# Kernel tuning notes

Measured on AMD Instinct MI355X. Metric: run time of the kernel, lower is better.

Reference implementation:

```python
import jax, jax.numpy as jnp
import numpy as np

B_, L_, DM = 2, 2048, 768        # batch, seq_len, d_model
DS, DC, EXP = 32, 7, 2           # d_state, d_conv, expand
DI = EXP * DM                    # d_inner = 1536
EPS = 1e-5


def setup_inputs() -> dict:
    key = jax.random.key(0)
    ks = jax.random.split(key, 6)
    sc = lambda k, shp: jax.random.normal(k, shp, jnp.float32) * 0.02
    x = jax.random.normal(ks[0], (B_, L_, DM), jnp.float32)
    Win = sc(ks[1], (2 * DI, DM))            # in_proj weight (no bias)
    conv_w = sc(ks[2], (DI, 1, DC))          # depthwise conv weight (O, I/groups, K)
    conv_b = jnp.zeros((DI,), jnp.float32)   # conv bias
    Wx = sc(ks[3], (2 * DS + DI, DI))        # x_proj weight (no bias)
    A_log = jnp.broadcast_to(jnp.log(jnp.arange(1, DS + 1, dtype=jnp.float32)), (DI, DS))
    D = jnp.ones((DI,), jnp.float32)
    Wout = sc(ks[4], (DM, DI))               # out_proj weight (no bias)
    ln_g = jnp.ones((DM,), jnp.float32)
    ln_b = jnp.zeros((DM,), jnp.float32)
    return {"x": x, "Win": Win, "conv_w": conv_w, "conv_b": conv_b, "Wx": Wx,
            "A_log": A_log, "D": D, "Wout": Wout, "ln_g": ln_g, "ln_b": ln_b}


def _mamba_forward(x, Win, conv_w, conv_b, Wx, A_log, D, Wout, ln_g, ln_b):
    residual = x
    # LayerNorm (biased variance, eps=1e-5)
    mu = jnp.mean(x, axis=-1, keepdims=True)
    var = jnp.var(x, axis=-1, keepdims=True)
    xn = (x - mu) / jnp.sqrt(var + EPS) * ln_g + ln_b
    # in_proj then split into x, z streams
    xz = xn @ Win.T                          # (b, l, 2*di)
    xc, z = jnp.split(xz, 2, axis=-1)
    # depthwise causal conv: pad (d_conv-1) left, truncate to L (matches torch pad+slice)
    xt = jnp.moveaxis(xc, 1, 2)              # (b, di, l)
    conv = jax.lax.conv_general_dilated(
        xt, conv_w, window_strides=(1,), padding=[(DC - 1, 0)],
        dimension_numbers=('NCH', 'OIH', 'NCH'), feature_group_count=DI)
    conv = conv + conv_b[None, :, None]
    xc = jax.nn.silu(jnp.moveaxis(conv, 1, 2))   # (b, l, di); dropout is identity (eval)
    # selective SSM
    xp = xc @ Wx.T                           # (b, l, 2*ds + di)
    Bm = xp[..., :DS]                        # (b, l, ds)
    Cm = xp[..., DS:2 * DS]                  # (b, l, ds)
    delta = jax.nn.softplus(xp[..., 2 * DS:])  # (b, l, di)
    A = -jnp.exp(A_log)                      # (di, ds)
    dA = jnp.exp(delta[..., None] * A)                       # (b, l, di, ds)
    dBx = (delta * xc)[..., None] * Bm[:, :, None, :]        # (b, l, di, ds)
    def step(h, inp):
        dA_t, dBx_t, C_t = inp
        h = dA_t * h + dBx_t                 # (b, di, ds)
        y = jnp.einsum('bdn,bn->bd', h, C_t)
        return h, y
    h0 = jnp.zeros((x.shape[0], DI, DS), xc.dtype)
    xs = (jnp.moveaxis(dA, 1, 0), jnp.moveaxis(dBx, 1, 0), jnp.moveaxis(Cm, 1, 0))
    _, ys = jax.lax.scan(step, h0, xs)       # (l, b, di)
    y = jnp.moveaxis(ys, 0, 1) + xc * D      # (b, l, di)
    # gated output, out_proj, residual
    y = y * jax.nn.silu(z)
    return y @ Wout.T + residual


def reference(x, Win, conv_w, conv_b, Wx, A_log, D, Wout, ln_g, ln_b):
    return _mamba_forward(x, Win, conv_w, conv_b, Wx, A_log, D, Wout, ln_g, ln_b)
```

## Files before the change

kernel.cpp:

```cpp
#include <hip/hip_runtime.h>
#include <hip/hip_bf16.h>

#define B_  2
#define L_  2048
#define DM  768
#define DS  32
#define DC  7
#define DI  1536
#define NTOK (B_*L_)
#define N1  (2*DI)
#define N2  (2*DS+DI)
#define N2P 1664
#define NC  64
#define CL  (L_/NC)
#define DGRP (DI/256)

using bf16 = __hip_bfloat16;
typedef short  short8 __attribute__((ext_vector_type(8)));
typedef short  s16x4  __attribute__((ext_vector_type(4)));
typedef float  f32x4  __attribute__((ext_vector_type(4)));
typedef unsigned u32x4 __attribute__((ext_vector_type(4)));

__device__ __forceinline__ float b2f(bf16 h) { return __bfloat162float(h); }
__device__ __forceinline__ bf16  f2b(float f){ return __float2bfloat16(f); }
__device__ __forceinline__ short bfbits(float f){ bf16 h = f2b(f); return *(short*)&h; }
__device__ __forceinline__ float bits2f(short s){ bf16 h; *(short*)&h = s; return b2f(h); }

__device__ __forceinline__ float exp2fast(float x) {
#if __has_builtin(__builtin_amdgcn_exp2f)
    return __builtin_amdgcn_exp2f(x);
#else
    return __expf(x * 0.6931471805599453f);
#endif
}

__global__ void detect_flag(const unsigned* __restrict__ lng, unsigned* __restrict__ flag)
{
    if (threadIdx.x == 0 && blockIdx.x == 0)
        *flag = (lng[0] == 0x3F800000u) ? 1u : 0u;
}

struct CvtArgs {
    const void* src[10];
    bf16*       dst[10];
    int         n[10];
    int         total;
};

__global__ __launch_bounds__(256) void convert_all(CvtArgs a, const unsigned* __restrict__ flag)
{
    int i = blockIdx.x * 256 + threadIdx.x;
    if (i >= a.total) return;
    int k = 0;
#pragma unroll
    for (int s = 0; s < 10; ++s) {
        if (i >= a.n[s]) { i -= a.n[s]; k = s + 1; }
        else break;
    }
    if (k >= 10) return;
    if (*flag) a.dst[k][i] = f2b(((const float*)a.src[k])[i]);
    else       a.dst[k][i] = ((const bf16*)a.src[k])[i];
}

__global__ __launch_bounds__(256) void ln_kernel(const bf16* __restrict__ x,
                                                 const bf16* __restrict__ g,
                                                 const bf16* __restrict__ b,
                                                 bf16* __restrict__ xn)
{
    int row = blockIdx.x;
    int t   = threadIdx.x;
    const bf16* xr = x + (size_t)row * DM;

    float v[3];
    float s = 0.f, s2 = 0.f;
#pragma unroll
    for (int i = 0; i < 3; ++i) {
        float f = b2f(xr[t + i * 256]);
        v[i] = f; s += f; s2 += f * f;
    }
#pragma unroll
    for (int off = 32; off > 0; off >>= 1) {
        s  += __shfl_down(s,  off);
        s2 += __shfl_down(s2, off);
    }
    __shared__ float red[8];
    if ((t & 63) == 0) { red[(t >> 6) * 2] = s; red[(t >> 6) * 2 + 1] = s2; }
    __syncthreads();
    float S  = red[0] + red[2] + red[4] + red[6];
    float S2 = red[1] + red[3] + red[5] + red[7];
    float mu  = S * (1.f / DM);
    float var = S2 * (1.f / DM) - mu * mu;
    float inv = 1.f / sqrtf(var + 1e-5f);
#pragma unroll
    for (int i = 0; i < 3; ++i) {
        int col = t + i * 256;
        float o = (v[i] - mu) * inv * b2f(g[col]) + b2f(b[col]);
        xn[(size_t)row * DM + col] = f2b(o);
    }
}

template<int MODE, int BN>
__global__ __launch_bounds__(256) void gemm_bt(const bf16* __restrict__ A,
                                               const bf16* __restrict__ W,
                                               void* __restrict__ Cout,
                                               const bf16* __restrict__ Res,
                                               int M, int N, int K, int LD,
                                               const unsigned* __restrict__ flag,
                                               bf16* __restrict__ BCb,
                                               bf16* __restrict__ dT)
{
    constexpr int BM = 128, BK = 32, PITCH = 40;
    constexpr int AU = BM * 4;
    constexpr int TU = (BM + BN) * 4;
    constexpr int NU = TU / 256;
    constexpr int MT = (BN == 128) ? 4 : 2;
    constexpr int NT = 4;
    __shared__ __align__(16) bf16 As[2][BM * PITCH];
    __shared__ __align__(16) bf16 Ws[2][BN * PITCH];

    int gx   = gridDim.x;
    int nwg  = gx * gridDim.y;
    int flat = blockIdx.y * gx + blockIdx.x;
    int swz  = (flat & 7) * (nwg >> 3) + (flat >> 3);
    int bx   = swz % gx, by = swz / gx;

    int kh = 0;
    if (MODE == 4) {
        int mblocks = M / BM;
        kh  = by / mblocks;
        by  = by % mblocks;
    }
    int koff = kh * K;

    int t    = threadIdx.x;
    int m0   = by * BM;
    int n0   = bx * BN;
    int wave = t >> 6, lane = t & 63;
    int quad = lane >> 4, l16 = lane & 15;
    int wm   = (BN == 128) ? (wave >> 1) * 64 : wave * 32;
    int wn   = (BN == 128) ? (wave & 1) * 64 : 0;

    auto loadu = [&](int u, int k0) -> short8 {
        if (u < AU) {
            int row = u >> 2, cu = (u & 3) * 8;
            return *(const short8*)(A + (size_t)(m0 + row) * LD + koff + k0 + cu);
        } else {
            int v = u - AU;
            int row = v >> 2, cu = (v & 3) * 8;
            int nrow = n0 + row;
            short8 z = {0,0,0,0,0,0,0,0};
            if (nrow < N) z = *(const short8*)(W + (size_t)nrow * LD + koff + k0 + cu);
            return z;
        }
    };
    auto storeu = [&](int buf, int u, short8 v) {
        if (u < AU) {
            int row = u >> 2, cu = (u & 3) * 8;
            *(short8*)(&As[buf][row * PITCH + cu]) = v;
        } else {
            int w = u - AU;
            int row = w >> 2, cu = (w & 3) * 8;
            *(short8*)(&Ws[buf][row * PITCH + cu]) = v;
        }
    };

    f32x4 acc[MT][NT] = {};
    short8 prA[NU], prB[NU];

#pragma unroll
    for (int p = 0; p < NU; ++p) prA[p] = loadu(t + 256 * p, 0);
#pragma unroll
    for (int p = 0; p < NU; ++p) storeu(0, t + 256 * p, prA[p]);
#pragma unroll
    for (int p = 0; p < NU; ++p) prB[p] = loadu(t + 256 * p, BK);
    __syncthreads();

    auto compute = [&](int buf) {
        short8 af[MT], bfr[NT];
#pragma unroll
        for (int i = 0; i < MT; ++i)
            af[i]  = *(const short8*)(&As[buf][(wm + i * 16 + l16) * PITCH + quad * 8]);
#pragma unroll
        for (int i = 0; i < NT; ++i)
            bfr[i] = *(const short8*)(&Ws[buf][(wn + i * 16 + l16) * PITCH + quad * 8]);
#pragma unroll
        for (int mt = 0; mt < MT; ++mt)
#pragma unroll
            for (int nt = 0; nt < NT; ++nt)
                acc[mt][nt] = __builtin_amdgcn_mfma_f32_16x16x32_bf16(
                    af[mt], bfr[nt], acc[mt][nt], 0, 0, 0);
    };

    for (int k0 = 0; k0 < K; k0 += 2 * BK) {
        if (k0 + 2 * BK < K) {
#pragma unroll
            for (int p = 0; p < NU; ++p) prA[p] = loadu(t + 256 * p, k0 + 2 * BK);
        }
        compute(0);
        {
#pragma unroll
            for (int p = 0; p < NU; ++p) storeu(1, t + 256 * p, prB[p]);
            __syncthreads();
        }
        if (k0 + 3 * BK < K) {
#pragma unroll
            for (int p = 0; p < NU; ++p) prB[p] = loadu(t + 256 * p, k0 + 3 * BK);
        }
        compute(1);
        if (k0 + 2 * BK < K) {
#pragma unroll
            for (int p = 0; p < NU; ++p) storeu(0, t + 256 * p, prA[p]);
            __syncthreads();
        }
    }

    bool f32out = (MODE == 2) ? (*flag != 0u) : false;

    if (MODE == 3) {
#pragma unroll
        for (int mt = 0; mt < MT; ++mt)
#pragma unroll
            for (int nt = 0; nt < NT; ++nt) {
                int row0 = m0 + wm + mt * 16 + quad * 4;
                int col  = n0 + wn + nt * 16 + l16;
                if (col >= N) continue;
                f32x4 v = acc[mt][nt];
                if (col < DS) {
#pragma unroll
                    for (int r = 0; r < 4; ++r)
                        BCb[(size_t)(row0 + r) * (2 * DS) + 2 * col] = f2b(v[r]);
                } else if (col < 2 * DS) {
#pragma unroll
                    for (int r = 0; r < 4; ++r)
                        BCb[(size_t)(row0 + r) * (2 * DS) + 2 * (col - DS) + 1] = f2b(v[r]);
                } else {
                    int dcol = col - 2 * DS;
#pragma unroll
                    for (int r = 0; r < 4; ++r) {
                        float x = v[r];
                        float s = fmaxf(x, 0.f) + __logf(1.f + __expf(-fabsf(x)));
                        dT[(size_t)(row0 + r) * DI + dcol] = f2b(s);
                    }
                }
            }
        return;
    }

    if (MODE == 4) {
        float* P = (float*)Cout + (size_t)kh * M * N;
#pragma unroll
        for (int mt = 0; mt < MT; ++mt)
#pragma unroll
            for (int nt = 0; nt < NT; ++nt)
#pragma unroll
                for (int r = 0; r < 4; ++r) {
                    int row = m0 + wm + mt * 16 + quad * 4 + r;
                    int col = n0 + wn + nt * 16 + l16;
                    P[(size_t)row * N + col] = acc[mt][nt][r];
                }
        return;
    }

#pragma unroll
    for (int mt = 0; mt < MT; ++mt)
#pragma unroll
        for (int nt = 0; nt < NT; ++nt)
#pragma unroll
            for (int r = 0; r < 4; ++r) {
                int row = m0 + wm + mt * 16 + quad * 4 + r;
                int col = n0 + wn + nt * 16 + l16;
                if (col >= N) continue;
                float v = acc[mt][nt][r];
                size_t idx = (size_t)row * N + col;
                if (MODE == 0) {
                    ((bf16*)Cout)[idx] = f2b(v);
                } else {
                    v += b2f(Res[idx]);
                    if (f32out) ((float*)Cout)[idx] = v;
                    else        ((bf16*)Cout)[idx]  = f2b(v);
                }
            }
}

__global__ __launch_bounds__(256) void reduce2(const float* __restrict__ p0,
                                               const float* __restrict__ p1,
                                               const bf16* __restrict__ res,
                                               void* __restrict__ out,
                                               const unsigned* __restrict__ flag,
                                               int n4)
{
    int i = blockIdx.x * 256 + threadIdx.x;
    if (i >= n4) return;
    f32x4 a = ((const f32x4*)p0)[i];
    f32x4 b = ((const f32x4*)p1)[i];
    s16x4 rz = ((const s16x4*)res)[i];
    f32x4 v;
#pragma unroll
    for (int j = 0; j < 4; ++j) v[j] = a[j] + b[j] + bits2f(rz[j]);
    if (*flag) {
        ((f32x4*)out)[i] = v;
    } else {
        s16x4 o;
#pragma unroll
        for (int j = 0; j < 4; ++j) o[j] = bfbits(v[j]);
        ((s16x4*)out)[i] = o;
    }
}

#define CCB 32
#define CTW 64
__global__ __launch_bounds__(256) void conv_silu(const bf16* __restrict__ xz,
                                                 const bf16* __restrict__ w,
                                                 const bf16* __restrict__ bias,
                                                 bf16* __restrict__ xconv)
{
    const int nCB = DI / CCB;
    int blk = blockIdx.x;
    int d0  = (blk % nCB) * CCB;
    int g0b = (blk / nCB) * CTW;
    int t   = threadIdx.x;
    int cb  = t & 31;
    int tg  = t >> 5;
    int d   = d0 + cb;
    int g0  = g0b + tg * 8;
    int l0  = g0 % L_;

    float wv[DC];
#pragma unroll
    for (int k = 0; k < DC; ++k) wv[k] = b2f(w[d * DC + k]);
    float bs = b2f(bias[d]);

    float xh[14];
#pragma unroll
    for (int j = 0; j < 14; ++j) {
        int lloc = l0 - 6 + j;
        xh[j] = (lloc >= 0) ? b2f(xz[(size_t)(g0 - 6 + j) * N1 + d]) : 0.f;
    }

#pragma unroll
    for (int r = 0; r < 8; ++r) {
        float acc = bs;
#pragma unroll
        for (int k = 0; k < DC; ++k)
            acc += xh[r + k] * wv[k];
        float s = acc / (1.f + __expf(-acc));
        xconv[(size_t)(g0 + r) * DI + d] = f2b(s);
    }
}

__global__ __launch_bounds__(256) void scan_a(const unsigned* __restrict__ BC32,
                                              const bf16* __restrict__ dT,
                                              const bf16* __restrict__ xc,
                                              const bf16* __restrict__ A_log,
                                              float* __restrict__ hend,
                                              float* __restrict__ sdbuf)
{
    int blk  = blockIdx.x;
    int dgrp = blk % DGRP;
    int bc   = blk / DGRP;
    int c    = bc % NC;
    int b    = bc / NC;
    int d    = dgrp * 256 + threadIdx.x;

    float a2[DS];
    {
        short8 al[4];
#pragma unroll
        for (int k = 0; k < 4; ++k) al[k] = *(const short8*)(A_log + d * DS + k * 8);
#pragma unroll
        for (int n = 0; n < DS; ++n)
            a2[n] = -__expf(bits2f(al[n >> 3][n & 7])) * 1.44269504f;
    }
    float h[DS];
#pragma unroll
    for (int n = 0; n < DS; ++n) h[n] = 0.f;
    float sd = 0.f;

    size_t tok0 = (size_t)b * L_ + (size_t)c * CL;
    for (int t = 0; t < CL; ++t) {
        size_t tok = tok0 + t;
        const u32x4* qp = (const u32x4*)(BC32 + tok * DS);
        u32x4 q[8];
#pragma unroll
        for (int k = 0; k < 8; ++k) q[k] = qp[k];
        float de = b2f(dT[tok * DI + d]);
        float xv = b2f(xc[tok * DI + d]);
        float w  = de * xv;
        sd += de;
#pragma unroll
        for (int n = 0; n < DS; ++n) {
            float Bn = __uint_as_float(q[n >> 2][n & 3] << 16);
            float dA = exp2fast(de * a2[n]);
            h[n] = fmaf(dA, h[n], w * Bn);
        }
    }
    size_t base = (size_t)bc * DS * DI + d;
#pragma unroll
    for (int n = 0; n < DS; ++n) hend[base + (size_t)n * DI] = h[n];
    sdbuf[(size_t)bc * DI + d] = sd;
}

__global__ __launch_bounds__(256) void scan_b(float* __restrict__ hend,
                                              const float* __restrict__ sdbuf,
                                              const bf16* __restrict__ A_log)
{
    int i = blockIdx.x * 256 + threadIdx.x;
    int d = i % DI;
    int r = i / DI;
    int n = r % DS;
    int b = r / DS;
    float a2 = -__expf(b2f(A_log[d * DS + n])) * 1.44269504f;
    float h = 0.f;
#pragma unroll 4
    for (int c = 0; c < NC; ++c) {
        int bc = b * NC + c;
        size_t idx = ((size_t)bc * DS + n) * DI + d;
        float he = hend[idx];
        float pa = exp2fast(a2 * sdbuf[(size_t)bc * DI + d]);
        hend[idx] = h;
        h = fmaf(pa, h, he);
    }
}

__global__ __launch_bounds__(256) void scan_c(const unsigned* __restrict__ BC32,
                                              const bf16* __restrict__ dT,
                                              const bf16* __restrict__ xc,
                                              const bf16* __restrict__ xz,
                                              const bf16* __restrict__ A_log,
                                              const bf16* __restrict__ Dp,
                                              const float* __restrict__ hin,
                                              bf16* __restrict__ yg)
{
    int blk  = blockIdx.x;
    int dgrp = blk % DGRP;
    int bc   = blk / DGRP;
    int c    = bc % NC;
    int b    = bc / NC;
    int d    = dgrp * 256 + threadIdx.x;

    float a2[DS];
    {
        short8 al[4];
#pragma unroll
        for (int k = 0; k < 4; ++k) al[k] = *(const short8*)(A_log + d * DS + k * 8);
#pragma unroll
        for (int n = 0; n < DS; ++n)
            a2[n] = -__expf(bits2f(al[n >> 3][n & 7])) * 1.44269504f;
    }
    float h[DS];
    size_t hb = (size_t)bc * DS * DI + d;
#pragma unroll
    for (int n = 0; n < DS; ++n) h[n] = hin[hb + (size_t)n * DI];
    float Dd = b2f(Dp[d]);

    size_t tok0 = (size_t)b * L_ + (size_t)c * CL;
    for (int t = 0; t < CL; ++t) {
        size_t tok = tok0 + t;
        const u32x4* qp = (const u32x4*)(BC32 + tok * DS);
        u32x4 q[8];
#pragma unroll
        for (int k = 0; k < 8; ++k) q[k] = qp[k];
        float de = b2f(dT[tok * DI + d]);
        float xv = b2f(xc[tok * DI + d]);
        float zf = b2f(xz[tok * N1 + DI + d]);
        float w  = de * xv;

        float ya[4] = {0.f, 0.f, 0.f, 0.f};
#pragma unroll
        for (int n = 0; n < DS; ++n) {
            unsigned dw = q[n >> 2][n & 3];
            float Bn  = __uint_as_float(dw << 16);
            float Cnv = __uint_as_float(dw & 0xFFFF0000u);
            float dA  = exp2fast(de * a2[n]);
            h[n] = fmaf(dA, h[n], w * Bn);
            ya[n & 3] = fmaf(h[n], Cnv, ya[n & 3]);
        }
        float y  = (ya[0] + ya[1]) + (ya[2] + ya[3]);
        float sz = zf / (1.f + __expf(-zf));
        yg[tok * DI + d] = f2b((y + xv * Dd) * sz);
    }
}

extern "C" void kernel_launch(void* const* d_in, const int* in_sizes, int n_in,
                              void* d_out, int out_size, void* d_ws, size_t ws_size,
                              hipStream_t stream)
{
    (void)in_sizes; (void)n_in; (void)out_size; (void)ws_size;

    char* ws = (char*)d_ws;
    size_t off = 0;
    auto alloc = [&](size_t bytes) -> char* {
        char* p = ws + off;
        off += (bytes + 255) & ~(size_t)255;
        return p;
    };

    unsigned* flag = (unsigned*)alloc(4);
    bf16*  xb     = (bf16*)alloc((size_t)NTOK * DM * 2);
    bf16*  Winb   = (bf16*)alloc((size_t)N1 * DM * 2);
    bf16*  convwb = (bf16*)alloc((size_t)DI * DC * 2);
    bf16*  convbb = (bf16*)alloc((size_t)DI * 2);
    bf16*  Wxb    = (bf16*)alloc((size_t)N2 * DI * 2);
    bf16*  Alogb  = (bf16*)alloc((size_t)DI * DS * 2);
    bf16*  Db     = (bf16*)alloc((size_t)DI * 2);
    bf16*  Woutb  = (bf16*)alloc((size_t)DM * DI * 2);
    bf16*  lngb   = (bf16*)alloc((size_t)DM * 2);
    bf16*  lnbb   = (bf16*)alloc((size_t)DM * 2);
    bf16*  xn     = (bf16*)alloc((size_t)NTOK * DM * 2);
    bf16*  xz     = (bf16*)alloc((size_t)NTOK * N1 * 2);
    bf16*  xconv  = (bf16*)alloc((size_t)NTOK * DI * 2);
    float* hend   = (float*)alloc((size_t)B_ * NC * DS * DI * 4);
    bf16*  BCb    = (bf16*)alloc((size_t)NTOK * 2 * DS * 2);
    bf16*  dTrm   = (bf16*)alloc((size_t)NTOK * DI * 2);
    bf16*  yg     = (bf16*)alloc((size_t)NTOK * DI * 2);
    float* sdbuf  = (float*)alloc((size_t)B_ * NC * DI * 4);
    float* g3p    = (float*)alloc((size_t)2 * NTOK * DM * 4);

    detect_flag<<<1, 64, 0, stream>>>((const unsigned*)d_in[8], flag);

    CvtArgs ca;
    const int ns[10] = { NTOK * DM, N1 * DM, DI * DC, DI, N2 * DI,
                         DI * DS, DI, DM * DI, DM, DM };
    bf16* ds[10] = { xb, Winb, convwb, convbb, Wxb, Alogb, Db, Woutb, lngb, lnbb };
    int total = 0;
    for (int k = 0; k < 10; ++k) {
        ca.src[k] = d_in[k];
        ca.dst[k] = ds[k];
        ca.n[k]   = ns[k];
        total    += ns[k];
    }
    ca.total = total;
    convert_all<<<(total + 255) / 256, 256, 0, stream>>>(ca, flag);

    ln_kernel<<<NTOK, 256, 0, stream>>>(xb, lngb, lnbb, xn);

    gemm_bt<0, 128><<<dim3(N1 / 128, NTOK / 128), 256, 0, stream>>>(
        xn, Winb, (void*)xz, nullptr, NTOK, N1, DM, DM, nullptr, nullptr, nullptr);

    conv_silu<<<(DI / CCB) * (NTOK / CTW), 256, 0, stream>>>(
        xz, convwb, convbb, xconv);

    gemm_bt<3, 128><<<dim3(N2P / 128, NTOK / 128), 256, 0, stream>>>(
        xconv, Wxb, nullptr, nullptr, NTOK, N2, DI, DI, nullptr, BCb, dTrm);

    scan_a<<<B_ * NC * DGRP, 256, 0, stream>>>(
        (const unsigned*)BCb, dTrm, xconv, Alogb, hend, sdbuf);
    scan_b<<<(B_ * DS * DI) / 256, 256, 0, stream>>>(hend, sdbuf, Alogb);
    scan_c<<<B_ * NC * DGRP, 256, 0, stream>>>(
        (const unsigned*)BCb, dTrm, xconv, xz, Alogb, Db, hend, yg);

    gemm_bt<4, 64><<<dim3(DM / 64, 2 * (NTOK / 128)), 256, 0, stream>>>(
        yg, Woutb, (void*)g3p, nullptr, NTOK, DM, DI / 2, DI, nullptr, nullptr, nullptr);
    reduce2<<<(NTOK * DM / 4 + 255) / 256, 256, 0, stream>>>(
        g3p, g3p + (size_t)NTOK * DM, xb, d_out, flag, NTOK * DM / 4);
}
```

Before: 342.7 us.

## Stage B/C in LDS as fp32 and prefetch next-step scan inputs

```diff
diff --git a/kernel.cpp b/kernel.cpp
--- a/kernel.cpp
+++ b/kernel.cpp
@@ -106,7 +106,7 @@
                                                const bf16* __restrict__ Res,
                                                int M, int N, int K, int LD,
                                                const unsigned* __restrict__ flag,
-                                               bf16* __restrict__ BCb,
+                                               float* __restrict__ BCf,
                                                bf16* __restrict__ dT)
 {
     constexpr int BM = 128, BK = 32, PITCH = 40;
@@ -217,6 +217,8 @@
     bool f32out = (MODE == 2) ? (*flag != 0u) : false;
 
     if (MODE == 3) {
+        float* Bf = BCf;
+        float* Cf = BCf + (size_t)NTOK * DS;
 #pragma unroll
         for (int mt = 0; mt < MT; ++mt)
 #pragma unroll
@@ -228,11 +230,11 @@
                 if (col < DS) {
 #pragma unroll
                     for (int r = 0; r < 4; ++r)
-                        BCb[(size_t)(row0 + r) * (2 * DS) + 2 * col] = f2b(v[r]);
+                        Bf[(size_t)(row0 + r) * DS + col] = v[r];
                 } else if (col < 2 * DS) {
 #pragma unroll
                     for (int r = 0; r < 4; ++r)
-                        BCb[(size_t)(row0 + r) * (2 * DS) + 2 * (col - DS) + 1] = f2b(v[r]);
+                        Cf[(size_t)(row0 + r) * DS + (col - DS)] = v[r];
                 } else {
                     int dcol = col - 2 * DS;
 #pragma unroll
@@ -348,7 +350,7 @@
     }
 }
 
-__global__ __launch_bounds__(256) void scan_a(const unsigned* __restrict__ BC32,
+__global__ __launch_bounds__(256) void scan_a(const float* __restrict__ Bf,
                                               const bf16* __restrict__ dT,
                                               const bf16* __restrict__ xc,
                                               const bf16* __restrict__ A_log,
@@ -362,6 +364,10 @@
     int b    = bc / NC;
     int d    = dgrp * 256 + threadIdx.x;
 
+    __shared__ float Bs[CL * DS];
+    size_t tok0 = (size_t)b * L_ + (size_t)c * CL;
+    ((f32x4*)Bs)[threadIdx.x] = ((const f32x4*)(Bf + tok0 * DS))[threadIdx.x];
+
     float a2[DS];
     {
         short8 al[4];
@@ -375,24 +381,25 @@
 #pragma unroll
     for (int n = 0; n < DS; ++n) h[n] = 0.f;
     float sd = 0.f;
-
-    size_t tok0 = (size_t)b * L_ + (size_t)c * CL;
+    __syncthreads();
+
+    float de_c = b2f(dT[tok0 * DI + d]);
+    float xv_c = b2f(xc[tok0 * DI + d]);
     for (int t = 0; t < CL; ++t) {
-        size_t tok = tok0 + t;
-        const u32x4* qp = (const u32x4*)(BC32 + tok * DS);
-        u32x4 q[8];
-#pragma unroll
-        for (int k = 0; k < 8; ++k) q[k] = qp[k];
-        float de = b2f(dT[tok * DI + d]);
-        float xv = b2f(xc[tok * DI + d]);
-        float w  = de * xv;
-        sd += de;
+        float de_n = de_c, xv_n = xv_c;
+        if (t + 1 < CL) {
+            de_n = b2f(dT[(tok0 + t + 1) * DI + d]);
+            xv_n = b2f(xc[(tok0 + t + 1) * DI + d]);
+        }
+        float w = de_c * xv_c;
+        sd += de_c;
 #pragma unroll
         for (int n = 0; n < DS; ++n) {
-            float Bn = __uint_as_float(q[n >> 2][n & 3] << 16);
-            float dA = exp2fast(de * a2[n]);
+            float Bn = Bs[t * DS + n];
+            float dA = exp2fast(de_c * a2[n]);
             h[n] = fmaf(dA, h[n], w * Bn);
         }
+        de_c = de_n; xv_c = xv_n;
     }
     size_t base = (size_t)bc * DS * DI + d;
 #pragma unroll
@@ -422,7 +429,8 @@
     }
 }
 
-__global__ __launch_bounds__(256) void scan_c(const unsigned* __restrict__ BC32,
+__global__ __launch_bounds__(256) void scan_c(const float* __restrict__ Bf,
+                                              const float* __restrict__ Cf,
                                               const bf16* __restrict__ dT,
                                               const bf16* __restrict__ xc,
                                               const bf16* __restrict__ xz,
@@ -438,6 +446,12 @@
     int b    = bc / NC;
     int d    = dgrp * 256 + threadIdx.x;
 
+    __shared__ float Bs[CL * DS];
+    __shared__ float Cs[CL * DS];
+    size_t tok0 = (size_t)b * L_ + (size_t)c * CL;
+    ((f32x4*)Bs)[threadIdx.x] = ((const f32x4*)(Bf + tok0 * DS))[threadIdx.x];
+    ((f32x4*)Cs)[threadIdx.x] = ((const f32x4*)(Cf + tok0 * DS))[threadIdx.x];
+
     float a2[DS];
     {
         short8 al[4];
@@ -452,32 +466,34 @@
 #pragma unroll
     for (int n = 0; n < DS; ++n) h[n] = hin[hb + (size_t)n * DI];
     float Dd = b2f(Dp[d]);
-
-    size_t tok0 = (size_t)b * L_ + (size_t)c * CL;
+    __syncthreads();
+
+    float de_c = b2f(dT[tok0 * DI + d]);
+    float xv_c = b2f(xc[tok0 * DI + d]);
+    float zf_c = b2f(xz[tok0 * N1 + DI + d]);
     for (int t = 0; t < CL; ++t) {
-        size_t tok = tok0 + t;
-        const u32x4* qp = (const u32x4*)(BC32 + tok * DS);
-        u32x4 q[8];
-#pragma unroll
-        for (int k = 0; k < 8; ++k) q[k] = qp[k];
-        float de = b2f(dT[tok * DI + d]);
-        float xv = b2f(xc[tok * DI + d]);
-        float zf = b2f(xz[tok * N1 + DI + d]);
-        float w  = de * xv;
+        float de_n = de_c, xv_n = xv_c, zf_n = zf_c;
+        if (t + 1 < CL) {
+            size_t tn = tok0 + t + 1;
+            de_n = b2f(dT[tn * DI + d]);
+            xv_n = b2f(xc[tn * DI + d]);
+            zf_n = b2f(xz[tn * N1 + DI + d]);
+        }
+        float w = de_c * xv_c;
 
         float ya[4] = {0.f, 0.f, 0.f, 0.f};
 #pragma unroll
         for (int n = 0; n < DS; ++n) {
-            unsigned dw = q[n >> 2][n & 3];
-            float Bn  = __uint_as_float(dw << 16);
-            float Cnv = __uint_as_float(dw & 0xFFFF0000u);
-            float dA  = exp2fast(de * a2[n]);
+            float Bn  = Bs[t * DS + n];
+            float Cnv = Cs[t * DS + n];
+            float dA  = exp2fast(de_c * a2[n]);
             h[n] = fmaf(dA, h[n], w * Bn);
             ya[n & 3] = fmaf(h[n], Cnv, ya[n & 3]);
         }
         float y  = (ya[0] + ya[1]) + (ya[2] + ya[3]);
-        float sz = zf / (1.f + __expf(-zf));
-        yg[tok * DI + d] = f2b((y + xv * Dd) * sz);
+        float sz = zf_c / (1.f + __expf(-zf_c));
+        yg[(tok0 + t) * DI + d] = f2b((y + xv_c * Dd) * sz);
+        de_c = de_n; xv_c = xv_n; zf_c = zf_n;
     }
 }
 
@@ -510,7 +526,7 @@
     bf16*  xz     = (bf16*)alloc((size_t)NTOK * N1 * 2);
     bf16*  xconv  = (bf16*)alloc((size_t)NTOK * DI * 2);
     float* hend   = (float*)alloc((size_t)B_ * NC * DS * DI * 4);
-    bf16*  BCb    = (bf16*)alloc((size_t)NTOK * 2 * DS * 2);
+    float* BCf    = (float*)alloc((size_t)2 * NTOK * DS * 4);
     bf16*  dTrm   = (bf16*)alloc((size_t)NTOK * DI * 2);
     bf16*  yg     = (bf16*)alloc((size_t)NTOK * DI * 2);
     float* sdbuf  = (float*)alloc((size_t)B_ * NC * DI * 4);
@@ -541,13 +557,13 @@
         xz, convwb, convbb, xconv);
 
     gemm_bt<3, 128><<<dim3(N2P / 128, NTOK / 128), 256, 0, stream>>>(
-        xconv, Wxb, nullptr, nullptr, NTOK, N2, DI, DI, nullptr, BCb, dTrm);
+        xconv, Wxb, nullptr, nullptr, NTOK, N2, DI, DI, nullptr, BCf, dTrm);
 
     scan_a<<<B_ * NC * DGRP, 256, 0, stream>>>(
-        (const unsigned*)BCb, dTrm, xconv, Alogb, hend, sdbuf);
+        BCf, dTrm, xconv, Alogb, hend, sdbuf);
     scan_b<<<(B_ * DS * DI) / 256, 256, 0, stream>>>(hend, sdbuf, Alogb);
     scan_c<<<B_ * NC * DGRP, 256, 0, stream>>>(
-        (const unsigned*)BCb, dTrm, xconv, xz, Alogb, Db, hend, yg);
+        BCf, BCf + (size_t)NTOK * DS, dTrm, xconv, xz, Alogb, Db, hend, yg);
 
     gemm_bt<4, 64><<<dim3(DM / 64, 2 * (NTOK / 128)), 256, 0, stream>>>(
         yg, Woutb, (void*)g3p, nullptr, NTOK, DM, DI / 2, DI, nullptr, nullptr, nullptr);
```

Result: no change. 336.2 us (-1.9%).
